# Kernel optimization log

Hardware: AMD Instinct MI355X
Metric: run time of the kernel (lower is better)

## Reference

```python
import jax, jax.numpy as jnp
import numpy as np

N_BUS = 1024
BATCH = 4096
N_NODES = N_BUS * BATCH
N_EDGES = 4 * N_NODES
F_IN, F1, F2, HID = 7, 12, 12, 128
EPS = 1e-5


def setup_inputs() -> dict:
    key = jax.random.key(0)
    ks = jax.random.split(key, 16)
    inp = {
        "x": jax.random.normal(ks[0], (N_NODES, F_IN), dtype=jnp.float32),
        "edge_index": jax.random.randint(ks[1], (2, N_EDGES), 0, N_NODES, dtype=jnp.int64),
        "batch_size": BATCH,
        # conv1 (PyG GraphConv): lin_rel (with bias) on aggregated msgs, lin_root (no bias)
        "Wrel1": jax.random.normal(ks[2], (F1, F_IN), dtype=jnp.float32) * 0.3,
        "brel1": jax.random.normal(ks[3], (F1,), dtype=jnp.float32) * 0.1,
        "Wroot1": jax.random.normal(ks[4], (F1, F_IN), dtype=jnp.float32) * 0.3,
        # conv2
        "Wrel2": jax.random.normal(ks[5], (F2, F1), dtype=jnp.float32) * 0.25,
        "brel2": jax.random.normal(ks[6], (F2,), dtype=jnp.float32) * 0.1,
        "Wroot2": jax.random.normal(ks[7], (F2, F1), dtype=jnp.float32) * 0.25,
        # batch norms
        "g1": jnp.ones((F1,), jnp.float32), "b1": jnp.zeros((F1,), jnp.float32),
        "g2": jnp.ones((F2,), jnp.float32), "b2": jnp.zeros((F2,), jnp.float32),
        # MLP head
        "W1": jax.random.normal(ks[8], (HID, N_BUS * F2), dtype=jnp.float32) * 0.01,
        "bl1": jnp.zeros((HID,), jnp.float32),
        "W2": jax.random.normal(ks[9], (N_BUS * 2, HID), dtype=jnp.float32) * 0.05,
        "bl2": jnp.zeros((N_BUS * 2,), jnp.float32),
    }
    return inp


def graph_conv(x, src, dst, Wrel, brel, Wroot):
    # out_i = Wrel @ (sum_{j: j->i} x_j) + brel + Wroot @ x_i
    agg = jax.ops.segment_sum(x[src], dst, num_segments=N_NODES)
    return agg @ Wrel.T + brel + x @ Wroot.T


def batch_norm(x, g, b):
    mu = x.mean(axis=0)
    var = x.var(axis=0)  # biased, as torch BN uses for normalization
    return (x - mu) * jax.lax.rsqrt(var + EPS) * g + b


def reference(x, edge_index, batch_size, Wrel1, brel1, Wroot1, Wrel2, brel2, Wroot2,
              g1, b1, g2, b2, W1, bl1, W2, bl2):
    src, dst = edge_index[0], edge_index[1]
    h = graph_conv(x, src, dst, Wrel1, brel1, Wroot1)
    h = jax.nn.relu(batch_norm(h, g1, b1))
    h = graph_conv(h, src, dst, Wrel2, brel2, Wroot2)
    h = jax.nn.relu(batch_norm(h, g2, b2))
    h = h.reshape(batch_size, N_BUS * F2)
    h = jax.nn.relu(h @ W1.T + bl1)
    return h @ W2.T + bl2
```

## Files before the change

### kernel.cpp

```cpp
#include <hip/hip_runtime.h>
#include <hip/hip_bf16.h>

#define NBUS    1024
#define BATCHSZ 4096
#define NNODES  (NBUS*BATCHSZ)
#define NEDGES  (4*NNODES)
#define FIN     7
#define FF1     12
#define FF2     12
#define HIDD    128
#define KDIM    (NBUS*FF2)
#define ODIM    (NBUS*2)
#define NBKT    4096
#define CAP     4608
#define NCB     64
#define CAPA    265216

#define SZ_P    ((size_t)NNODES * 32)
#define SZ_HB   ((size_t)NNODES * FF2 * 2)
#define SZ_HID  ((size_t)BATCHSZ * HIDD * sizeof(float))
#define SZ_E    ((size_t)NBKT * CAP * sizeof(unsigned))
#define SZ_PB   ((size_t)NCB * CAPA * 8)
#define SZ_W1B  ((size_t)HIDD * KDIM * 2)

typedef unsigned u32x2v  __attribute__((ext_vector_type(2)));
typedef unsigned u32x4v  __attribute__((ext_vector_type(4)));
typedef __attribute__((ext_vector_type(8))) short bf16x8;
typedef __attribute__((ext_vector_type(4))) float f32x4;

__device__ __forceinline__ float bflo(unsigned p){ return __uint_as_float(p << 16); }
__device__ __forceinline__ float bfhi(unsigned p){ return __uint_as_float(p & 0xffff0000u); }
__device__ __forceinline__ unsigned short f2bf(float f) {
    unsigned u = __float_as_uint(f);
    return (unsigned short)((u + 0x7fffu + ((u >> 16) & 1u)) >> 16);
}
__device__ __forceinline__ void nts_u2(unsigned* p, unsigned a, unsigned b) {
    u32x2v w; w.x = a; w.y = b;
    __builtin_nontemporal_store(w, (u32x2v*)p);
}
__device__ __forceinline__ void nts_u4(uint4* p, uint4 v) {
    u32x4v w; w.x = v.x; w.y = v.y; w.z = v.z; w.w = v.w;
    __builtin_nontemporal_store(w, (u32x4v*)p);
}
__device__ __forceinline__ uint2 ntl_u2(const unsigned* p) {
    u32x2v v = __builtin_nontemporal_load((const u32x2v*)p);
    uint2 r; r.x = v.x; r.y = v.y; return r;
}

__device__ __forceinline__ void acc7(float* agg, uint4 a) {
    agg[0] += bflo(a.x); agg[1] += bfhi(a.x);
    agg[2] += bflo(a.y); agg[3] += bfhi(a.y);
    agg[4] += bflo(a.z); agg[5] += bfhi(a.z);
    agg[6] += bflo(a.w);
}
__device__ __forceinline__ void accY(float* agg, const float* sc, const float* sh,
                                     uint4 r0, uint4 r1) {
    float v[FF1] = {bflo(r0.x), bfhi(r0.x), bflo(r0.y), bfhi(r0.y),
                    bflo(r0.z), bfhi(r0.z), bflo(r0.w), bfhi(r0.w),
                    bflo(r1.x), bfhi(r1.x), bflo(r1.y), bfhi(r1.y)};
    #pragma unroll
    for (int j = 0; j < FF1; ++j) {
        float y = v[j] * sc[j] + sh[j];
        agg[j] += (y > 0.f ? y : 0.f);
    }
}

__global__ void k_diag(float* __restrict__ out, int n, float v) {
    size_t i = (size_t)blockIdx.x * blockDim.x + threadIdx.x;
    if (i < (size_t)n) out[i] = v;
}

__global__ void k_init(const int* __restrict__ w, int* __restrict__ flag,
                       int* __restrict__ bcur, int* __restrict__ bcurA) {
    int u = blockIdx.x * 256 + threadIdx.x;
    if (u < NBKT) bcur[u] = u * CAP;
    if (u < NCB) bcurA[u] = u * CAPA;
    if (blockIdx.x == 0) {
        __shared__ int any;
        if (threadIdx.x == 0) any = 0;
        __syncthreads();
        int acc = 0;
        #pragma unroll
        for (int q = 0; q < 4; ++q) acc |= w[1 + 2 * (threadIdx.x * 4 + q)];
        if (acc) atomicOr(&any, 1);
        __syncthreads();
        if (threadIdx.x == 0) *flag = (any == 0) ? 2 : 1;
    }
}

__global__ __launch_bounds__(512) void k_partA(const int* __restrict__ ei,
                                               const int* __restrict__ flag,
                                               int* __restrict__ bcurA,
                                               unsigned* __restrict__ ebufA) {
    __shared__ int hist[8][NCB];
    __shared__ int lbase[8][NCB];
    int t = threadIdx.x;
    int w8 = t >> 6;
    for (int u = t; u < 8 * NCB; u += 512) ((int*)hist)[u] = 0;
    __syncthreads();
    int mult = *flag;
    size_t base = (size_t)blockIdx.x * 32768;
    #pragma unroll 4
    for (int u = 0; u < 64; ++u) {
        size_t e = base + (size_t)u * 512 + t;
        int d = __builtin_nontemporal_load(ei + ((size_t)NEDGES + e) * mult);
        atomicAdd(&hist[w8][d >> 16], 1);
    }
    __syncthreads();
    if (t < NCB) {
        int c[8]; int ctot = 0;
        #pragma unroll
        for (int ww = 0; ww < 8; ++ww) { c[ww] = hist[ww][t]; ctot += c[ww]; }
        int bg = ctot ? atomicAdd(&bcurA[t], ctot) : 0;
        #pragma unroll
        for (int ww = 0; ww < 8; ++ww) { lbase[ww][t] = bg; bg += c[ww]; hist[ww][t] = 0; }
    }
    __syncthreads();
    #pragma unroll 4
    for (int u = 0; u < 64; ++u) {
        size_t e = base + (size_t)u * 512 + t;
        int s = __builtin_nontemporal_load(ei + e * mult);
        int d = __builtin_nontemporal_load(ei + ((size_t)NEDGES + e) * mult);
        int bk = d >> 16;
        int pos = lbase[w8][bk] + atomicAdd(&hist[w8][bk], 1);
        if (pos < (bk + 1) * CAPA) {
            uint2* p = (uint2*)(ebufA + (size_t)pos * 2);
            *p = make_uint2((unsigned)s, (unsigned)d);
        }
    }
}

__global__ __launch_bounds__(512) void k_partB(const unsigned* __restrict__ ebufA,
                                               const int* __restrict__ bendA,
                                               int* __restrict__ bcur,
                                               unsigned* __restrict__ ebuf) {
    __shared__ int hist[8][NCB];
    __shared__ int lbase[8][NCB];
    int t = threadIdx.x;
    int w8 = t >> 6;
    int cb = blockIdx.x >> 2;
    int qq = blockIdx.x & 3;
    int abeg = cb * CAPA;
    int n = bendA[cb] - abeg; if (n > CAPA) n = CAPA;
    int beg = abeg + (int)(((long long)n * qq) >> 2);
    int end = abeg + (int)(((long long)n * (qq + 1)) >> 2);
    for (int u = t; u < 8 * NCB; u += 512) ((int*)hist)[u] = 0;
    __syncthreads();
    for (int k = beg + t; k < end; k += 512) {
        uint2 e = ntl_u2(ebufA + (size_t)k * 2);
        atomicAdd(&hist[w8][(e.y >> 10) & 63u], 1);
    }
    __syncthreads();
    if (t < NCB) {
        int c[8]; int ctot = 0;
        #pragma unroll
        for (int ww = 0; ww < 8; ++ww) { c[ww] = hist[ww][t]; ctot += c[ww]; }
        int bg = ctot ? atomicAdd(&bcur[cb * 64 + t], ctot) : 0;
        #pragma unroll
        for (int ww = 0; ww < 8; ++ww) { lbase[ww][t] = bg; bg += c[ww]; hist[ww][t] = 0; }
    }
    __syncthreads();
    for (int k = beg + t; k < end; k += 512) {
        uint2 e = ntl_u2(ebufA + (size_t)k * 2);
        int lb = (e.y >> 10) & 63u;
        int fb = cb * 64 + lb;
        int pos = lbase[w8][lb] + atomicAdd(&hist[w8][lb], 1);
        if (pos < (fb + 1) * CAP)
            ebuf[pos] = (e.x << 10) | (e.y & 1023u);
    }
}

__global__ __launch_bounds__(256) void k_padx(const float* __restrict__ x,
                                              uint4* __restrict__ xb) {
    size_t q = (size_t)blockIdx.x * blockDim.x + threadIdx.x;
    if (q >= NNODES / 4) return;
    const float4* xr = (const float4*)(x + q * 28);
    float v[28];
    #pragma unroll
    for (int u = 0; u < 7; ++u) {
        float4 f = xr[u];
        v[4*u] = f.x; v[4*u+1] = f.y; v[4*u+2] = f.z; v[4*u+3] = f.w;
    }
    #pragma unroll
    for (int n = 0; n < 4; ++n) {
        unsigned short h[8];
        #pragma unroll
        for (int j = 0; j < 7; ++j) h[j] = f2bf(v[7*n + j]);
        h[7] = 0;
        uint4 o;
        o.x = (unsigned)h[0] | ((unsigned)h[1] << 16);
        o.y = (unsigned)h[2] | ((unsigned)h[3] << 16);
        o.z = (unsigned)h[4] | ((unsigned)h[5] << 16);
        o.w = (unsigned)h[6] | ((unsigned)h[7] << 16);
        xb[q * 4 + n] = o;
    }
}

__global__ __launch_bounds__(256) void k_w1b(const float* __restrict__ W1,
                                             uint4* __restrict__ w1b) {
    size_t q = (size_t)blockIdx.x * blockDim.x + threadIdx.x;
    if (q >= (size_t)HIDD * KDIM / 8) return;
    const float4* r = (const float4*)(W1 + q * 8);
    float4 a = r[0], b = r[1];
    uint4 o;
    o.x = (unsigned)f2bf(a.x) | ((unsigned)f2bf(a.y) << 16);
    o.y = (unsigned)f2bf(a.z) | ((unsigned)f2bf(a.w) << 16);
    o.z = (unsigned)f2bf(b.x) | ((unsigned)f2bf(b.y) << 16);
    o.w = (unsigned)f2bf(b.z) | ((unsigned)f2bf(b.w) << 16);
    w1b[q] = o;
}

__global__ __launch_bounds__(256, 4) void k_conv1(const int* __restrict__ bend,
                                                  const unsigned* __restrict__ ebuf,
                                                  const uint4* __restrict__ xb,
                                                  const float* __restrict__ Wrel,
                                                  const float* __restrict__ brel,
                                                  const float* __restrict__ Wroot,
                                                  uint4* __restrict__ h1p) {
    __shared__ unsigned stage[CAP];
    __shared__ int hist[1024];
    __shared__ int offL[1024];
    __shared__ int wsum[4];
    __shared__ float sWr[FF1 * FIN], sWo[FF1 * FIN], sb[FF1];
    int t = threadIdx.x;
    if (t < FF1 * FIN) { sWr[t] = Wrel[t]; sWo[t] = Wroot[t]; }
    if (t < FF1) sb[t] = brel[t];
    int bk = blockIdx.x;
    int ebeg = bk * CAP;
    int n = bend[bk] - ebeg; if (n > CAP) n = CAP; if (n < 0) n = 0;
    for (int u = t; u < 1024; u += 256) hist[u] = 0;
    __syncthreads();
    for (int k = t; k < n; k += 256)
        atomicAdd(&hist[ebuf[ebeg + k] & 1023u], 1);
    __syncthreads();
    int v[4]; int s = 0;
    #pragma unroll
    for (int u = 0; u < 4; ++u) { v[u] = hist[t * 4 + u]; s += v[u]; }
    int lane = t & 63, w = t >> 6;
    int iv = s;
    for (int o = 1; o < 64; o <<= 1) { int uu = __shfl_up(iv, o); if (lane >= o) iv += uu; }
    if (lane == 63) wsum[w] = iv;
    __syncthreads();
    int basep = 0;
    #pragma unroll
    for (int ww = 0; ww < 4; ++ww) if (ww < w) basep += wsum[ww];
    int run = basep + iv - s;
    #pragma unroll
    for (int u = 0; u < 4; ++u) {
        offL[t * 4 + u] = run;
        hist[t * 4 + u] = run;
        run += v[u];
    }
    __syncthreads();
    for (int k = t; k < n; k += 256) {
        unsigned p = ebuf[ebeg + k];
        int pos = atomicAdd(&hist[p & 1023u], 1);
        stage[pos] = p >> 10;
    }
    __syncthreads();
    #pragma unroll
    for (int nn = 0; nn < 4; ++nn) {
        int li = nn * 256 + t;
        size_t i = (size_t)bk * 1024 + li;
        int beg = offL[li];
        int end = (li == 1023) ? n : offL[li + 1];
        float agg[FIN] = {0.f, 0.f, 0.f, 0.f, 0.f, 0.f, 0.f};
        int k = beg;
        for (; k + 3 < end; k += 4) {
            unsigned s0 = stage[k], s1 = stage[k+1], s2 = stage[k+2], s3 = stage[k+3];
            uint4 a0 = xb[s0], a1 = xb[s1], a2 = xb[s2], a3 = xb[s3];
            acc7(agg, a0); acc7(agg, a1); acc7(agg, a2); acc7(agg, a3);
        }
        for (; k < end; ++k) acc7(agg, xb[stage[k]]);
        uint4 ow = xb[i];
        float xv[FIN] = {bflo(ow.x), bfhi(ow.x), bflo(ow.y), bfhi(ow.y),
                         bflo(ow.z), bfhi(ow.z), bflo(ow.w)};
        unsigned short hh[FF1];
        #pragma unroll
        for (int j = 0; j < FF1; ++j) {
            float h = sb[j];
            #pragma unroll
            for (int q = 0; q < FIN; ++q) h += sWr[j * FIN + q] * agg[q] + sWo[j * FIN + q] * xv[q];
            hh[j] = f2bf(h);
        }
        uint4 w1, w2;
        w1.x = (unsigned)hh[0] | ((unsigned)hh[1] << 16);
        w1.y = (unsigned)hh[2] | ((unsigned)hh[3] << 16);
        w1.z = (unsigned)hh[4] | ((unsigned)hh[5] << 16);
        w1.w = (unsigned)hh[6] | ((unsigned)hh[7] << 16);
        w2.x = (unsigned)hh[8] | ((unsigned)hh[9] << 16);
        w2.y = (unsigned)hh[10]| ((unsigned)hh[11] << 16);
        w2.z = 0u; w2.w = 0u;
        nts_u4(h1p + i * 2, w1);
        nts_u4(h1p + i * 2 + 1, w2);
    }
}

template<int STRIDE>
__global__ __launch_bounds__(256) void k_statsb(const unsigned* __restrict__ hb,
                                                double* __restrict__ stats) {
    __shared__ float red[4][FF1], redq[4][FF1];
    int t = threadIdx.x;
    float ps[FF1], pq[FF1];
    #pragma unroll
    for (int j = 0; j < FF1; ++j) { ps[j] = 0.f; pq[j] = 0.f; }
    for (size_t i = (size_t)blockIdx.x * 256 + t; i < NNODES; i += 256 * 256) {
        const uint2* r = (const uint2*)(hb + i * STRIDE);
        uint2 u0 = r[0], u1 = r[1], u2 = r[2];
        float v[FF1] = {bflo(u0.x), bfhi(u0.x), bflo(u0.y), bfhi(u0.y),
                        bflo(u1.x), bfhi(u1.x), bflo(u1.y), bfhi(u1.y),
                        bflo(u2.x), bfhi(u2.x), bflo(u2.y), bfhi(u2.y)};
        #pragma unroll
        for (int j = 0; j < FF1; ++j) { ps[j] += v[j]; pq[j] += v[j] * v[j]; }
    }
    #pragma unroll
    for (int j = 0; j < FF1; ++j)
        for (int o = 1; o < 64; o <<= 1) { ps[j] += __shfl_xor(ps[j], o); pq[j] += __shfl_xor(pq[j], o); }
    int lane = t & 63, wv = t >> 6;
    if (lane == 0) {
        #pragma unroll
        for (int j = 0; j < FF1; ++j) { red[wv][j] = ps[j]; redq[wv][j] = pq[j]; }
    }
    __syncthreads();
    if (t < FF1) {
        float s = red[0][t] + red[1][t] + red[2][t] + red[3][t];
        float q = redq[0][t] + redq[1][t] + redq[2][t] + redq[3][t];
        atomicAdd(&stats[t], (double)s);
        atomicAdd(&stats[FF1 + t], (double)q);
    }
}

__global__ void k_finalize(const double* __restrict__ stats, const float* __restrict__ g,
                           const float* __restrict__ b, float* __restrict__ ss) {
    int j = threadIdx.x;
    if (j < FF1) {
        double mean = stats[j] * (1.0 / NNODES);
        double var  = stats[FF1 + j] * (1.0 / NNODES) - mean * mean;
        float sc = (float)((double)g[j] / sqrt(var + 1e-5));
        ss[j] = sc;
        ss[FF1 + j] = b[j] - (float)mean * sc;
    }
}

__global__ __launch_bounds__(256, 4) void k_conv2(const int* __restrict__ bend,
                                                  const unsigned* __restrict__ ebuf,
                                                  const uint4* __restrict__ h1p,
                                                  const float* __restrict__ ss,
                                                  const float* __restrict__ Wrel,
                                                  const float* __restrict__ brel,
                                                  const float* __restrict__ Wroot,
                                                  unsigned* __restrict__ h2b) {
    __shared__ unsigned stage[CAP];
    __shared__ int hist[1024];
    __shared__ int offL[1024];
    __shared__ int wsum[4];
    __shared__ float sWr[FF2 * FF1], sWo[FF2 * FF1], sb[FF2], sc[FF1], sh[FF1];
    int t = threadIdx.x;
    if (t < FF2 * FF1) { sWr[t] = Wrel[t]; sWo[t] = Wroot[t]; }
    if (t < FF2) { sb[t] = brel[t]; sc[t] = ss[t]; sh[t] = ss[FF1 + t]; }
    int bk = blockIdx.x;
    int ebeg = bk * CAP;
    int n = bend[bk] - ebeg; if (n > CAP) n = CAP; if (n < 0) n = 0;
    for (int u = t; u < 1024; u += 256) hist[u] = 0;
    __syncthreads();
    for (int k = t; k < n; k += 256)
        atomicAdd(&hist[ebuf[ebeg + k] & 1023u], 1);
    __syncthreads();
    int v[4]; int s = 0;
    #pragma unroll
    for (int u = 0; u < 4; ++u) { v[u] = hist[t * 4 + u]; s += v[u]; }
    int lane = t & 63, w = t >> 6;
    int iv = s;
    for (int o = 1; o < 64; o <<= 1) { int uu = __shfl_up(iv, o); if (lane >= o) iv += uu; }
    if (lane == 63) wsum[w] = iv;
    __syncthreads();
    int basep = 0;
    #pragma unroll
    for (int ww = 0; ww < 4; ++ww) if (ww < w) basep += wsum[ww];
    int run = basep + iv - s;
    #pragma unroll
    for (int u = 0; u < 4; ++u) {
        offL[t * 4 + u] = run;
        hist[t * 4 + u] = run;
        run += v[u];
    }
    __syncthreads();
    for (int k = t; k < n; k += 256) {
        unsigned p = ebuf[ebeg + k];
        int pos = atomicAdd(&hist[p & 1023u], 1);
        stage[pos] = p >> 10;
    }
    __syncthreads();
    #pragma unroll
    for (int nn = 0; nn < 4; ++nn) {
        int li = nn * 256 + t;
        size_t i = (size_t)bk * 1024 + li;
        int beg = offL[li];
        int end = (li == 1023) ? n : offL[li + 1];
        float agg[FF1];
        #pragma unroll
        for (int j = 0; j < FF1; ++j) agg[j] = 0.f;
        int k = beg;
        for (; k + 3 < end; k += 4) {
            unsigned s0 = stage[k], s1 = stage[k+1], s2 = stage[k+2], s3 = stage[k+3];
            uint4 a0 = h1p[(size_t)s0 * 2], a1 = h1p[(size_t)s0 * 2 + 1];
            uint4 b0 = h1p[(size_t)s1 * 2], b1 = h1p[(size_t)s1 * 2 + 1];
            uint4 c0 = h1p[(size_t)s2 * 2], c1 = h1p[(size_t)s2 * 2 + 1];
            uint4 d0 = h1p[(size_t)s3 * 2], d1 = h1p[(size_t)s3 * 2 + 1];
            accY(agg, sc, sh, a0, a1);
            accY(agg, sc, sh, b0, b1);
            accY(agg, sc, sh, c0, c1);
            accY(agg, sc, sh, d0, d1);
        }
        for (; k < end; ++k) {
            unsigned s0 = stage[k];
            accY(agg, sc, sh, h1p[(size_t)s0 * 2], h1p[(size_t)s0 * 2 + 1]);
        }
        uint4 o0 = h1p[i * 2], o1 = h1p[i * 2 + 1];
        float vo[FF1] = {bflo(o0.x), bfhi(o0.x), bflo(o0.y), bfhi(o0.y),
                         bflo(o0.z), bfhi(o0.z), bflo(o0.w), bfhi(o0.w),
                         bflo(o1.x), bfhi(o1.x), bflo(o1.y), bfhi(o1.y)};
        float y[FF1];
        #pragma unroll
        for (int j = 0; j < FF1; ++j) {
            float wv = vo[j] * sc[j] + sh[j];
            y[j] = wv > 0.f ? wv : 0.f;
        }
        unsigned short hh[FF2];
        #pragma unroll
        for (int j = 0; j < FF2; ++j) {
            float h = sb[j];
            #pragma unroll
            for (int q = 0; q < FF1; ++q) h += sWr[j * FF1 + q] * agg[q] + sWo[j * FF1 + q] * y[q];
            hh[j] = f2bf(h);
        }
        unsigned* p = h2b + i * 6;
        nts_u2(p,     (unsigned)hh[0] | ((unsigned)hh[1] << 16),
                      (unsigned)hh[2] | ((unsigned)hh[3] << 16));
        nts_u2(p + 2, (unsigned)hh[4] | ((unsigned)hh[5] << 16),
                      (unsigned)hh[6] | ((unsigned)hh[7] << 16));
        nts_u2(p + 4, (unsigned)hh[8] | ((unsigned)hh[9] << 16),
                      (unsigned)hh[10]| ((unsigned)hh[11] << 16));
    }
}

__global__ __launch_bounds__(256) void k_gemm1m(const unsigned short* __restrict__ h2b,
                                                const float* __restrict__ ss2,
                                                const unsigned short* __restrict__ w1b,
                                                float* __restrict__ hidp) {
    __shared__ float sc[FF2], sh[FF2];
    int t = threadIdx.x;
    if (t < FF2) { sc[t] = ss2[t]; sh[t] = ss2[FF2 + t]; }
    __syncthreads();
    const int KS = KDIM / 8;
    int mb = blockIdx.x;
    int ks = blockIdx.y;
    int wid = t >> 6;
    int lane = t & 63;
    int wm = wid >> 1, wn = wid & 1;
    int m0 = mb * 128 + wm * 64;
    int n0 = wn * 64;
    int lrow = lane & 15;
    int kgrp = lane >> 4;
    f32x4 acc[4][4];
    #pragma unroll
    for (int mi = 0; mi < 4; ++mi)
        #pragma unroll
        for (int ni = 0; ni < 4; ++ni) acc[mi][ni] = (f32x4)(0.f);
    int kbase = ks * KS;
    for (int k0 = 0; k0 < KS; k0 += 32) {
        int kk = kbase + k0 + kgrp * 8;
        bf16x8 af[4], bf[4];
        #pragma unroll
        for (int mi = 0; mi < 4; ++mi) {
            const unsigned short* ap = h2b + (size_t)(m0 + mi * 16 + lrow) * KDIM + kk;
            uint4 av = *(const uint4*)ap;
            unsigned hw[8] = {av.x & 0xffffu, av.x >> 16, av.y & 0xffffu, av.y >> 16,
                              av.z & 0xffffu, av.z >> 16, av.w & 0xffffu, av.w >> 16};
            int j = kk % FF2;
            bf16x8 r;
            #pragma unroll
            for (int u = 0; u < 8; ++u) {
                float f = __uint_as_float(hw[u] << 16);
                float y = f * sc[j] + sh[j];
                y = y > 0.f ? y : 0.f;
                r[u] = (short)f2bf(y);
                ++j; if (j >= FF2) j = 0;
            }
            af[mi] = r;
        }
        #pragma unroll
        for (int ni = 0; ni < 4; ++ni)
            bf[ni] = *(const bf16x8*)(w1b + (size_t)(n0 + ni * 16 + lrow) * KDIM + kk);
        #pragma unroll
        for (int mi = 0; mi < 4; ++mi)
            #pragma unroll
            for (int ni = 0; ni < 4; ++ni)
                acc[mi][ni] = __builtin_amdgcn_mfma_f32_16x16x32_bf16(
                    af[mi], bf[ni], acc[mi][ni], 0, 0, 0);
    }
    float* obase = hidp + (size_t)ks * (BATCHSZ * HIDD);
    #pragma unroll
    for (int mi = 0; mi < 4; ++mi) {
        #pragma unroll
        for (int ni = 0; ni < 4; ++ni) {
            #pragma unroll
            for (int reg = 0; reg < 4; ++reg) {
                int row = m0 + mi * 16 + kgrp * 4 + reg;
                int col = n0 + ni * 16 + lrow;
                obase[(size_t)row * HIDD + col] = acc[mi][ni][reg];
            }
        }
    }
}

__global__ __launch_bounds__(256) void k_hred(const float* __restrict__ hidp,
                                              const float* __restrict__ bl1,
                                              float* __restrict__ hid) {
    int i = blockIdx.x * 256 + threadIdx.x;
    float s = bl1[i & (HIDD - 1)];
    #pragma unroll
    for (int p = 0; p < 8; ++p) s += hidp[(size_t)p * (BATCHSZ * HIDD) + i];
    hid[i] = s > 0.f ? s : 0.f;
}

__global__ __launch_bounds__(256) void k_gemm2(const float* __restrict__ hid,
                                               const float* __restrict__ W2,
                                               const float* __restrict__ bl2,
                                               float* __restrict__ out) {
    __shared__ float As[32][128];
    __shared__ float Bs[32][128];
    int t = threadIdx.x;
    int m0 = blockIdx.x * 128;
    int n0 = blockIdx.y * 128;
    int r  = t >> 1;
    int kg = t & 1;
    int tr = t >> 4;
    int tc = t & 15;
    float acc[8][8];
    #pragma unroll
    for (int i = 0; i < 8; ++i)
        #pragma unroll
        for (int j = 0; j < 8; ++j) acc[i][j] = 0.f;

    for (int kt = 0; kt < HIDD; kt += 32) {
        int c0 = kt + 16 * kg;
        #pragma unroll
        for (int i = 0; i < 4; ++i) {
            float4 av = *(const float4*)(hid + (size_t)(m0 + r) * HIDD + c0 + 4 * i);
            As[16 * kg + 4 * i + 0][r] = av.x;
            As[16 * kg + 4 * i + 1][r] = av.y;
            As[16 * kg + 4 * i + 2][r] = av.z;
            As[16 * kg + 4 * i + 3][r] = av.w;
            float4 bv = *(const float4*)(W2 + (size_t)(n0 + r) * HIDD + c0 + 4 * i);
            Bs[16 * kg + 4 * i + 0][r] = bv.x;
            Bs[16 * kg + 4 * i + 1][r] = bv.y;
            Bs[16 * kg + 4 * i + 2][r] = bv.z;
            Bs[16 * kg + 4 * i + 3][r] = bv.w;
        }
        __syncthreads();
        #pragma unroll
        for (int k = 0; k < 32; ++k) {
            float a[8], b[8];
            *(float4*)&a[0] = *(const float4*)&As[k][8 * tr];
            *(float4*)&a[4] = *(const float4*)&As[k][8 * tr + 4];
            *(float4*)&b[0] = *(const float4*)&Bs[k][8 * tc];
            *(float4*)&b[4] = *(const float4*)&Bs[k][8 * tc + 4];
            #pragma unroll
            for (int i = 0; i < 8; ++i)
                #pragma unroll
                for (int j = 0; j < 8; ++j) acc[i][j] += a[i] * b[j];
        }
        __syncthreads();
    }
    float4 c0v = *(const float4*)(bl2 + n0 + 8 * tc);
    float4 c1v = *(const float4*)(bl2 + n0 + 8 * tc + 4);
    float bvals[8] = {c0v.x, c0v.y, c0v.z, c0v.w, c1v.x, c1v.y, c1v.z, c1v.w};
    #pragma unroll
    for (int i = 0; i < 8; ++i) {
        size_t ro = (size_t)(m0 + 8 * tr + i) * ODIM + n0 + 8 * tc;
        *(float4*)(out + ro)     = make_float4(acc[i][0] + bvals[0], acc[i][1] + bvals[1],
                                               acc[i][2] + bvals[2], acc[i][3] + bvals[3]);
        *(float4*)(out + ro + 4) = make_float4(acc[i][4] + bvals[4], acc[i][5] + bvals[5],
                                               acc[i][6] + bvals[6], acc[i][7] + bvals[7]);
    }
}

extern "C" void kernel_launch(void* const* d_in, const int* in_sizes, int n_in,
                              void* d_out, int out_size, void* d_ws, size_t ws_size,
                              hipStream_t stream) {
    const float* x      = (const float*)d_in[0];
    const int*   ei     = (const int*)d_in[1];
    const float* Wrel1  = (const float*)d_in[3];
    const float* brel1  = (const float*)d_in[4];
    const float* Wroot1 = (const float*)d_in[5];
    const float* Wrel2  = (const float*)d_in[6];
    const float* brel2  = (const float*)d_in[7];
    const float* Wroot2 = (const float*)d_in[8];
    const float* g1     = (const float*)d_in[9];
    const float* b1     = (const float*)d_in[10];
    const float* g2     = (const float*)d_in[11];
    const float* b2     = (const float*)d_in[12];
    const float* W1     = (const float*)d_in[13];
    const float* bl1    = (const float*)d_in[14];
    const float* W2     = (const float*)d_in[15];
    const float* bl2    = (const float*)d_in[16];
    float* out = (float*)d_out;
    char* ws = (char*)d_ws;

    const size_t req = SZ_P + SZ_E + SZ_PB + 32768 + SZ_W1B;
    if (ws_size < req) {
        float v = (float)(ws_size >> 20);
        k_diag<<<(out_size + 255) / 256, 256, 0, stream>>>(out, out_size, v);
        return;
    }
    char* pY = ws;
    unsigned* ebuf = (unsigned*)(ws + SZ_P);
    char* pB = ws + SZ_P + SZ_E;
    char* pK = ws + SZ_P + SZ_E + SZ_PB;
    int*  bcur  = (int*)pK;
    int*  bcurA = (int*)(pK + 16384);
    char* smalls = pK + 20480;
    double* st1  = (double*)smalls;
    double* st2  = st1 + 2 * FF1;
    float*  ss1  = (float*)(st2 + 2 * FF2);
    float*  ss2  = ss1 + 2 * FF1;
    int*    flag = (int*)(ss2 + 2 * FF2);
    uint4*  w1b  = (uint4*)(pK + 32768);

    uint4*    xb    = (uint4*)pY;
    unsigned* h2b   = (unsigned*)pY;
    float*    hidp  = (float*)(pY + SZ_HB);
    float*    hid   = (float*)(pY + SZ_HB + 8 * SZ_HID);
    unsigned* ebufA = (unsigned*)pB;
    uint4*    h1p   = (uint4*)pB;

    hipMemsetAsync(smalls, 0, 1024, stream);
    k_init  <<<16, 256, 0, stream>>>(ei, flag, bcur, bcurA);
    k_padx  <<<NNODES / 4 / 256, 256, 0, stream>>>(x, xb);
    k_w1b   <<<HIDD * KDIM / 8 / 256, 256, 0, stream>>>(W1, w1b);
    k_partA <<<512, 512, 0, stream>>>(ei, flag, bcurA, ebufA);
    k_partB <<<NCB * 4, 512, 0, stream>>>(ebufA, bcurA, bcur, ebuf);
    k_conv1 <<<NBKT, 256, 0, stream>>>(bcur, ebuf, xb, Wrel1, brel1, Wroot1, h1p);
    k_statsb<8><<<256, 256, 0, stream>>>((const unsigned*)h1p, st1);
    k_finalize<<<1, 64, 0, stream>>>(st1, g1, b1, ss1);
    k_conv2 <<<NBKT, 256, 0, stream>>>(bcur, ebuf, h1p, ss1, Wrel2, brel2, Wroot2, h2b);
    k_statsb<6><<<256, 256, 0, stream>>>(h2b, st2);
    k_finalize<<<1, 64, 0, stream>>>(st2, g2, b2, ss2);
    k_gemm1m<<<dim3(BATCHSZ / 128, 8), 256, 0, stream>>>((const unsigned short*)h2b, ss2,
                                                         (const unsigned short*)w1b, hidp);
    k_hred <<<BATCHSZ * HIDD / 256, 256, 0, stream>>>(hidp, bl1, hid);
    k_gemm2<<<dim3(BATCHSZ / 128, ODIM / 128), 256, 0, stream>>>(hid, W2, bl2, out);
}
```

Measured before the change: 1.384 ms.

## Replace global-atomic bucket partitioning with fixed per-block edge segments

```diff
diff --git a/kernel.cpp b/kernel.cpp
--- a/kernel.cpp
+++ b/kernel.cpp
@@ -12,15 +12,17 @@
 #define KDIM    (NBUS*FF2)
 #define ODIM    (NBUS*2)
 #define NBKT    4096
-#define CAP     4608
 #define NCB     64
-#define CAPA    265216
+#define NBLKA   512
+#define CAPW    648
+#define CAPQ    1216
+#define STCAP   4864
 
 #define SZ_P    ((size_t)NNODES * 32)
 #define SZ_HB   ((size_t)NNODES * FF2 * 2)
 #define SZ_HID  ((size_t)BATCHSZ * HIDD * sizeof(float))
-#define SZ_E    ((size_t)NBKT * CAP * sizeof(unsigned))
-#define SZ_PB   ((size_t)NCB * CAPA * 8)
+#define SZ_E    ((size_t)NBKT * 4 * CAPQ * 4)
+#define SZ_A    ((size_t)NCB * NBLKA * CAPW * 8)
 #define SZ_W1B  ((size_t)HIDD * KDIM * 2)
 
 typedef unsigned u32x2v  __attribute__((ext_vector_type(2)));
@@ -70,104 +72,72 @@
     if (i < (size_t)n) out[i] = v;
 }
 
-__global__ void k_init(const int* __restrict__ w, int* __restrict__ flag,
-                       int* __restrict__ bcur, int* __restrict__ bcurA) {
-    int u = blockIdx.x * 256 + threadIdx.x;
-    if (u < NBKT) bcur[u] = u * CAP;
-    if (u < NCB) bcurA[u] = u * CAPA;
-    if (blockIdx.x == 0) {
-        __shared__ int any;
-        if (threadIdx.x == 0) any = 0;
-        __syncthreads();
-        int acc = 0;
-        #pragma unroll
-        for (int q = 0; q < 4; ++q) acc |= w[1 + 2 * (threadIdx.x * 4 + q)];
-        if (acc) atomicOr(&any, 1);
-        __syncthreads();
-        if (threadIdx.x == 0) *flag = (any == 0) ? 2 : 1;
-    }
+__global__ void k_init(const int* __restrict__ w, int* __restrict__ flag) {
+    __shared__ int any;
+    if (threadIdx.x == 0) any = 0;
+    __syncthreads();
+    int acc = 0;
+    #pragma unroll
+    for (int q = 0; q < 4; ++q) acc |= w[1 + 2 * (threadIdx.x * 4 + q)];
+    if (acc) atomicOr(&any, 1);
+    __syncthreads();
+    if (threadIdx.x == 0) *flag = (any == 0) ? 2 : 1;
 }
 
 __global__ __launch_bounds__(512) void k_partA(const int* __restrict__ ei,
                                                const int* __restrict__ flag,
-                                               int* __restrict__ bcurA,
-                                               unsigned* __restrict__ ebufA) {
-    __shared__ int hist[8][NCB];
-    __shared__ int lbase[8][NCB];
+                                               unsigned* __restrict__ ebufA,
+                                               int* __restrict__ bcntA) {
+    __shared__ int lcnt[NCB];
     int t = threadIdx.x;
-    int w8 = t >> 6;
-    for (int u = t; u < 8 * NCB; u += 512) ((int*)hist)[u] = 0;
+    if (t < NCB) lcnt[t] = 0;
     __syncthreads();
     int mult = *flag;
-    size_t base = (size_t)blockIdx.x * 32768;
-    #pragma unroll 4
-    for (int u = 0; u < 64; ++u) {
-        size_t e = base + (size_t)u * 512 + t;
-        int d = __builtin_nontemporal_load(ei + ((size_t)NEDGES + e) * mult);
-        atomicAdd(&hist[w8][d >> 16], 1);
-    }
-    __syncthreads();
-    if (t < NCB) {
-        int c[8]; int ctot = 0;
-        #pragma unroll
-        for (int ww = 0; ww < 8; ++ww) { c[ww] = hist[ww][t]; ctot += c[ww]; }
-        int bg = ctot ? atomicAdd(&bcurA[t], ctot) : 0;
-        #pragma unroll
-        for (int ww = 0; ww < 8; ++ww) { lbase[ww][t] = bg; bg += c[ww]; hist[ww][t] = 0; }
-    }
-    __syncthreads();
+    int blk = blockIdx.x;
+    size_t base = (size_t)blk * 32768;
     #pragma unroll 4
     for (int u = 0; u < 64; ++u) {
         size_t e = base + (size_t)u * 512 + t;
         int s = __builtin_nontemporal_load(ei + e * mult);
         int d = __builtin_nontemporal_load(ei + ((size_t)NEDGES + e) * mult);
-        int bk = d >> 16;
-        int pos = lbase[w8][bk] + atomicAdd(&hist[w8][bk], 1);
-        if (pos < (bk + 1) * CAPA) {
-            uint2* p = (uint2*)(ebufA + (size_t)pos * 2);
+        int cb = d >> 16;
+        int pos = atomicAdd(&lcnt[cb], 1);
+        if (pos < CAPW) {
+            uint2* p = (uint2*)(ebufA + ((size_t)(cb * NBLKA + blk) * CAPW + pos) * 2);
             *p = make_uint2((unsigned)s, (unsigned)d);
         }
     }
+    __syncthreads();
+    if (t < NCB) bcntA[t * NBLKA + blk] = lcnt[t] > CAPW ? CAPW : lcnt[t];
 }
 
 __global__ __launch_bounds__(512) void k_partB(const unsigned* __restrict__ ebufA,
-                                               const int* __restrict__ bendA,
-                                               int* __restrict__ bcur,
-                                               unsigned* __restrict__ ebuf) {
-    __shared__ int hist[8][NCB];
-    __shared__ int lbase[8][NCB];
+                                               const int* __restrict__ bcntA,
+                                               unsigned* __restrict__ ebuf,
+                                               int* __restrict__ bcntB) {
+    __shared__ int lcnt[NCB];
+    __shared__ int scnt[128];
     int t = threadIdx.x;
-    int w8 = t >> 6;
     int cb = blockIdx.x >> 2;
-    int qq = blockIdx.x & 3;
-    int abeg = cb * CAPA;
-    int n = bendA[cb] - abeg; if (n > CAPA) n = CAPA;
-    int beg = abeg + (int)(((long long)n * qq) >> 2);
-    int end = abeg + (int)(((long long)n * (qq + 1)) >> 2);
-    for (int u = t; u < 8 * NCB; u += 512) ((int*)hist)[u] = 0;
-    __syncthreads();
-    for (int k = beg + t; k < end; k += 512) {
-        uint2 e = ntl_u2(ebufA + (size_t)k * 2);
-        atomicAdd(&hist[w8][(e.y >> 10) & 63u], 1);
-    }
-    __syncthreads();
-    if (t < NCB) {
-        int c[8]; int ctot = 0;
-        #pragma unroll
-        for (int ww = 0; ww < 8; ++ww) { c[ww] = hist[ww][t]; ctot += c[ww]; }
-        int bg = ctot ? atomicAdd(&bcur[cb * 64 + t], ctot) : 0;
-        #pragma unroll
-        for (int ww = 0; ww < 8; ++ww) { lbase[ww][t] = bg; bg += c[ww]; hist[ww][t] = 0; }
-    }
-    __syncthreads();
-    for (int k = beg + t; k < end; k += 512) {
-        uint2 e = ntl_u2(ebufA + (size_t)k * 2);
-        int lb = (e.y >> 10) & 63u;
-        int fb = cb * 64 + lb;
-        int pos = lbase[w8][lb] + atomicAdd(&hist[w8][lb], 1);
-        if (pos < (fb + 1) * CAP)
-            ebuf[pos] = (e.x << 10) | (e.y & 1023u);
-    }
+    int q  = blockIdx.x & 3;
+    if (t < NCB) lcnt[t] = 0;
+    if (t < 128) scnt[t] = bcntA[cb * NBLKA + q * 128 + t];
+    __syncthreads();
+    for (int b = 0; b < 128; ++b) {
+        int blk = q * 128 + b;
+        int n = scnt[b];
+        const unsigned* seg = ebufA + (size_t)(cb * NBLKA + blk) * CAPW * 2;
+        for (int k = t; k < n; k += 512) {
+            uint2 e = ntl_u2(seg + (size_t)k * 2);
+            int lb = (e.y >> 10) & 63;
+            int pos = atomicAdd(&lcnt[lb], 1);
+            if (pos < CAPQ)
+                ebuf[((size_t)((cb * 64 + lb) * 4) + q) * CAPQ + pos] =
+                    (e.x << 10) | (e.y & 1023u);
+        }
+    }
+    __syncthreads();
+    if (t < NCB) bcntB[(cb * 64 + t) * 4 + q] = lcnt[t] > CAPQ ? CAPQ : lcnt[t];
 }
 
 __global__ __launch_bounds__(256) void k_padx(const float* __restrict__ x,
@@ -210,14 +180,14 @@
     w1b[q] = o;
 }
 
-__global__ __launch_bounds__(256, 4) void k_conv1(const int* __restrict__ bend,
+__global__ __launch_bounds__(256, 4) void k_conv1(const int* __restrict__ bcntB,
                                                   const unsigned* __restrict__ ebuf,
                                                   const uint4* __restrict__ xb,
                                                   const float* __restrict__ Wrel,
                                                   const float* __restrict__ brel,
                                                   const float* __restrict__ Wroot,
                                                   uint4* __restrict__ h1p) {
-    __shared__ unsigned stage[CAP];
+    __shared__ unsigned stage[STCAP];
     __shared__ int hist[1024];
     __shared__ int offL[1024];
     __shared__ int wsum[4];
@@ -226,12 +196,17 @@
     if (t < FF1 * FIN) { sWr[t] = Wrel[t]; sWo[t] = Wroot[t]; }
     if (t < FF1) sb[t] = brel[t];
     int bk = blockIdx.x;
-    int ebeg = bk * CAP;
-    int n = bend[bk] - ebeg; if (n > CAP) n = CAP; if (n < 0) n = 0;
+    int nq[4]; int ntot = 0;
+    #pragma unroll
+    for (int q = 0; q < 4; ++q) { nq[q] = bcntB[bk * 4 + q]; ntot += nq[q]; }
     for (int u = t; u < 1024; u += 256) hist[u] = 0;
     __syncthreads();
-    for (int k = t; k < n; k += 256)
-        atomicAdd(&hist[ebuf[ebeg + k] & 1023u], 1);
+    #pragma unroll
+    for (int q = 0; q < 4; ++q) {
+        const unsigned* seg = ebuf + ((size_t)bk * 4 + q) * CAPQ;
+        for (int k = t; k < nq[q]; k += 256)
+            atomicAdd(&hist[seg[k] & 1023u], 1);
+    }
     __syncthreads();
     int v[4]; int s = 0;
     #pragma unroll
@@ -252,10 +227,14 @@
         run += v[u];
     }
     __syncthreads();
-    for (int k = t; k < n; k += 256) {
-        unsigned p = ebuf[ebeg + k];
-        int pos = atomicAdd(&hist[p & 1023u], 1);
-        stage[pos] = p >> 10;
+    #pragma unroll
+    for (int q = 0; q < 4; ++q) {
+        const unsigned* seg = ebuf + ((size_t)bk * 4 + q) * CAPQ;
+        for (int k = t; k < nq[q]; k += 256) {
+            unsigned p = seg[k];
+            int pos = atomicAdd(&hist[p & 1023u], 1);
+            stage[pos] = p >> 10;
+        }
     }
     __syncthreads();
     #pragma unroll
@@ -263,7 +242,7 @@
         int li = nn * 256 + t;
         size_t i = (size_t)bk * 1024 + li;
         int beg = offL[li];
-        int end = (li == 1023) ? n : offL[li + 1];
+        int end = (li == 1023) ? ntot : offL[li + 1];
         float agg[FIN] = {0.f, 0.f, 0.f, 0.f, 0.f, 0.f, 0.f};
         int k = beg;
         for (; k + 3 < end; k += 4) {
@@ -342,7 +321,7 @@
     }
 }
 
-__global__ __launch_bounds__(256, 4) void k_conv2(const int* __restrict__ bend,
+__global__ __launch_bounds__(256, 4) void k_conv2(const int* __restrict__ bcntB,
                                                   const unsigned* __restrict__ ebuf,
                                                   const uint4* __restrict__ h1p,
                                                   const float* __restrict__ ss,
@@ -350,7 +329,7 @@
                                                   const float* __restrict__ brel,
                                                   const float* __restrict__ Wroot,
                                                   unsigned* __restrict__ h2b) {
-    __shared__ unsigned stage[CAP];
+    __shared__ unsigned stage[STCAP];
     __shared__ int hist[1024];
     __shared__ int offL[1024];
     __shared__ int wsum[4];
@@ -359,12 +338,17 @@
     if (t < FF2 * FF1) { sWr[t] = Wrel[t]; sWo[t] = Wroot[t]; }
     if (t < FF2) { sb[t] = brel[t]; sc[t] = ss[t]; sh[t] = ss[FF1 + t]; }
     int bk = blockIdx.x;
-    int ebeg = bk * CAP;
-    int n = bend[bk] - ebeg; if (n > CAP) n = CAP; if (n < 0) n = 0;
+    int nq[4]; int ntot = 0;
+    #pragma unroll
+    for (int q = 0; q < 4; ++q) { nq[q] = bcntB[bk * 4 + q]; ntot += nq[q]; }
     for (int u = t; u < 1024; u += 256) hist[u] = 0;
     __syncthreads();
-    for (int k = t; k < n; k += 256)
-        atomicAdd(&hist[ebuf[ebeg + k] & 1023u], 1);
+    #pragma unroll
+    for (int q = 0; q < 4; ++q) {
+        const unsigned* seg = ebuf + ((size_t)bk * 4 + q) * CAPQ;
+        for (int k = t; k < nq[q]; k += 256)
+            atomicAdd(&hist[seg[k] & 1023u], 1);
+    }
     __syncthreads();
     int v[4]; int s = 0;
     #pragma unroll
@@ -385,10 +369,14 @@
         run += v[u];
     }
     __syncthreads();
-    for (int k = t; k < n; k += 256) {
-        unsigned p = ebuf[ebeg + k];
-        int pos = atomicAdd(&hist[p & 1023u], 1);
-        stage[pos] = p >> 10;
+    #pragma unroll
+    for (int q = 0; q < 4; ++q) {
+        const unsigned* seg = ebuf + ((size_t)bk * 4 + q) * CAPQ;
+        for (int k = t; k < nq[q]; k += 256) {
+            unsigned p = seg[k];
+            int pos = atomicAdd(&hist[p & 1023u], 1);
+            stage[pos] = p >> 10;
+        }
     }
     __syncthreads();
     #pragma unroll
@@ -396,7 +384,7 @@
         int li = nn * 256 + t;
         size_t i = (size_t)bk * 1024 + li;
         int beg = offL[li];
-        int end = (li == 1023) ? n : offL[li + 1];
+        int end = (li == 1023) ? ntot : offL[li + 1];
         float agg[FF1];
         #pragma unroll
         for (int j = 0; j < FF1; ++j) agg[j] = 0.f;
@@ -608,7 +596,7 @@
     float* out = (float*)d_out;
     char* ws = (char*)d_ws;
 
-    const size_t req = SZ_P + SZ_E + SZ_PB + 32768 + SZ_W1B;
+    const size_t req = SZ_P + SZ_E + SZ_A + 262144 + SZ_W1B;
     if (ws_size < req) {
         float v = (float)(ws_size >> 20);
         k_diag<<<(out_size + 255) / 256, 256, 0, stream>>>(out, out_size, v);
@@ -617,16 +605,16 @@
     char* pY = ws;
     unsigned* ebuf = (unsigned*)(ws + SZ_P);
     char* pB = ws + SZ_P + SZ_E;
-    char* pK = ws + SZ_P + SZ_E + SZ_PB;
-    int*  bcur  = (int*)pK;
-    int*  bcurA = (int*)(pK + 16384);
-    char* smalls = pK + 20480;
+    char* pK = ws + SZ_P + SZ_E + SZ_A;
+    int*  bcntA = (int*)pK;
+    int*  bcntB = (int*)(pK + 131072);
+    char* smalls = pK + 131072 + 65536;
     double* st1  = (double*)smalls;
     double* st2  = st1 + 2 * FF1;
     float*  ss1  = (float*)(st2 + 2 * FF2);
     float*  ss2  = ss1 + 2 * FF1;
     int*    flag = (int*)(ss2 + 2 * FF2);
-    uint4*  w1b  = (uint4*)(pK + 32768);
+    uint4*  w1b  = (uint4*)(pK + 131072 + 65536 + 4096);
 
     uint4*    xb    = (uint4*)pY;
     unsigned* h2b   = (unsigned*)pY;
@@ -636,15 +624,15 @@
     uint4*    h1p   = (uint4*)pB;
 
     hipMemsetAsync(smalls, 0, 1024, stream);
-    k_init  <<<16, 256, 0, stream>>>(ei, flag, bcur, bcurA);
+    k_init  <<<1, 256, 0, stream>>>(ei, flag);
     k_padx  <<<NNODES / 4 / 256, 256, 0, stream>>>(x, xb);
     k_w1b   <<<HIDD * KDIM / 8 / 256, 256, 0, stream>>>(W1, w1b);
-    k_partA <<<512, 512, 0, stream>>>(ei, flag, bcurA, ebufA);
-    k_partB <<<NCB * 4, 512, 0, stream>>>(ebufA, bcurA, bcur, ebuf);
-    k_conv1 <<<NBKT, 256, 0, stream>>>(bcur, ebuf, xb, Wrel1, brel1, Wroot1, h1p);
+    k_partA <<<NBLKA, 512, 0, stream>>>(ei, flag, ebufA, bcntA);
+    k_partB <<<NCB * 4, 512, 0, stream>>>(ebufA, bcntA, ebuf, bcntB);
+    k_conv1 <<<NBKT, 256, 0, stream>>>(bcntB, ebuf, xb, Wrel1, brel1, Wroot1, h1p);
     k_statsb<8><<<256, 256, 0, stream>>>((const unsigned*)h1p, st1);
     k_finalize<<<1, 64, 0, stream>>>(st1, g1, b1, ss1);
-    k_conv2 <<<NBKT, 256, 0, stream>>>(bcur, ebuf, h1p, ss1, Wrel2, brel2, Wroot2, h2b);
+    k_conv2 <<<NBKT, 256, 0, stream>>>(bcntB, ebuf, h1p, ss1, Wrel2, brel2, Wroot2, h2b);
     k_statsb<6><<<256, 256, 0, stream>>>(h2b, st2);
     k_finalize<<<1, 64, 0, stream>>>(st2, g2, b2, ss2);
     k_gemm1m<<<dim3(BATCHSZ / 128, 8), 256, 0, stream>>>((const unsigned short*)h2b, ss2,
```

New measurement: 1.188 ms. 1.16x faster.
